# Optimization experiments

Measured on AMD Instinct MI355X. Metric: run time of the kernel, lower is better.

Reference implementation:

```python
import jax, jax.numpy as jnp
import numpy as np

N_NODES = 50000


def gcn_conv(x, src, dst, deg_inv_sqrt, W, b, n_nodes):
    # GCNConv: h = x @ W; msg = norm * h[src]; out = scatter_add(msg, dst) + b
    h = x @ W  # [N, out]
    norm = deg_inv_sqrt[src] * deg_inv_sqrt[dst]  # symmetric normalization
    msg = h[src] * norm[:, None]  # [E+N, out]
    out = jax.ops.segment_sum(msg, dst, num_segments=n_nodes)
    return out + b


def setup_inputs() -> dict:
    key = jax.random.key(0)
    k_x, k_e, k_w1, k_w2 = jax.random.split(key, 4)
    in_c, hid, out_c = 256, 64, 64
    x = jax.random.normal(k_x, (N_NODES, 256), dtype=jnp.float32)
    edge_index = jax.random.randint(k_e, (2, 1600000), 0, N_NODES, dtype=jnp.int64)
    # Glorot-ish weights, zero bias as in GCNConv defaults
    W1 = jax.random.normal(k_w1, (in_c, hid), dtype=jnp.float32) / np.sqrt(in_c)
    b1 = jnp.zeros((hid,), dtype=jnp.float32)
    W2 = jax.random.normal(k_w2, (hid, out_c), dtype=jnp.float32) / np.sqrt(hid)
    b2 = jnp.zeros((out_c,), dtype=jnp.float32)
    return {"x": x, "edge_index": edge_index, "W1": W1, "b1": b1, "W2": W2, "b2": b2}


def reference(x, edge_index, W1, b1, W2, b2):
    n = x.shape[0]
    loops = jnp.arange(n, dtype=edge_index.dtype)
    src = jnp.concatenate([edge_index[0], loops])  # add self-loops
    dst = jnp.concatenate([edge_index[1], loops])
    deg = jax.ops.segment_sum(jnp.ones_like(dst, dtype=x.dtype), dst, num_segments=n)
    deg_inv_sqrt = jnp.where(deg > 0, jax.lax.rsqrt(deg), 0.0)
    h = gcn_conv(x, src, dst, deg_inv_sqrt, W1, b1, n)
    h = jax.nn.relu(h)
    out = gcn_conv(h, src, dst, deg_inv_sqrt, W2, b2, n)
    return out
```

## Files before the change

### kernel.cpp

```cpp
#include <hip/hip_runtime.h>
#include <hip/hip_bf16.h>


#define NB_MAX 1024

__device__ inline unsigned short f2bf(float f) {
    unsigned u = __builtin_bit_cast(unsigned, f);
    return (unsigned short)((u + 0x7FFFu + ((u >> 16) & 1u)) >> 16);
}
__device__ inline float bf2f(unsigned short b) {
    return __builtin_bit_cast(float, (unsigned)b << 16);
}


__global__ __launch_bounds__(256) void k_hist(const int* __restrict__ ei, int E,
                                              int nb, int chunk,
                                              int* __restrict__ histT) {
    __shared__ int h[NB_MAX];
    for (int i = threadIdx.x; i < nb; i += 256) h[i] = 0;
    __syncthreads();
    int e0 = blockIdx.x * chunk, e1 = min(E, e0 + chunk);
    for (int e = e0 + threadIdx.x; e < e1; e += 256)
        atomicAdd(&h[ei[E + e] >> 6], 1);
    __syncthreads();
    for (int b = threadIdx.x; b < nb; b += 256)
        histT[b * 256 + blockIdx.x] = h[b];
}


__global__ __launch_bounds__(256) void k_scan_cols(int* __restrict__ histT,
                                                   int* __restrict__ total) {
    __shared__ int sm[256];
    int b = blockIdx.x, t = threadIdx.x;
    int v = histT[b * 256 + t];
    sm[t] = v;
    __syncthreads();
    for (int off = 1; off < 256; off <<= 1) {
        int u = (t >= off) ? sm[t - off] : 0;
        __syncthreads();
        sm[t] += u;
        __syncthreads();
    }
    histT[b * 256 + t] = sm[t] - v;
    if (t == 255) total[b] = sm[255];
}


__global__ __launch_bounds__(1024) void k_scan_totals(const int* __restrict__ total,
                                                      int* __restrict__ base, int nb) {
    __shared__ int sm[1024];
    int t = threadIdx.x;
    int v = (t < nb) ? total[t] : 0;
    sm[t] = v;
    __syncthreads();
    for (int off = 1; off < 1024; off <<= 1) {
        int u = (t >= off) ? sm[t - off] : 0;
        __syncthreads();
        sm[t] += u;
        __syncthreads();
    }
    if (t < nb) base[t] = sm[t] - v;
    if (t == nb - 1) base[nb] = sm[t];
}


__global__ __launch_bounds__(256) void k_scatter(const int* __restrict__ ei, int E,
                                                 int nb, int chunk,
                                                 const int* __restrict__ histT,
                                                 const int* __restrict__ base,
                                                 unsigned* __restrict__ packed) {
    __shared__ int cur[NB_MAX];
    for (int b = threadIdx.x; b < nb; b += 256)
        cur[b] = base[b] + histT[b * 256 + blockIdx.x];
    __syncthreads();
    int e0 = blockIdx.x * chunk, e1 = min(E, e0 + chunk);
    for (int e = e0 + threadIdx.x; e < e1; e += 256) {
        int s = ei[e], d = ei[E + e];
        int pos = atomicAdd(&cur[d >> 6], 1);
        packed[pos] = (unsigned)s | ((unsigned)(d & 63) << 16);
    }
}


__global__ __launch_bounds__(256) void k_csr(const unsigned* __restrict__ packed,
                                             const int* __restrict__ base,
                                             int n,
                                             int* __restrict__ qbeg,
                                             int* __restrict__ qcnt,
                                             float* __restrict__ dinv,
                                             unsigned short* __restrict__ ssrcp,
                                             unsigned short* __restrict__ hs1,
                                             unsigned short* __restrict__ hs2) {
    __shared__ int cnt[64];
    __shared__ int cur[64];
    const int b = blockIdx.x, t = threadIdx.x;
    const int p0 = base[b], p1 = base[b + 1];
    if (t < 64) cnt[t] = 0;
    __syncthreads();
    for (int p = p0 + t; p < p1; p += 256)
        atomicAdd(&cnt[(packed[p] >> 16) & 63], 1);
    __syncthreads();
    if (t < 64) {
        int deg = cnt[t];
        int pdeg = (deg + 1) & ~1;
        int sum = pdeg;
#pragma unroll
        for (int d = 1; d < 64; d <<= 1) {
            int u = __shfl_up(sum, d, 64);
            if (t >= d) sum += u;
        }
        int excl = sum - pdeg;
        int pb = (2 + p0 + 128 * b + 1) & ~1;
        int start = pb + excl;
        int node = (b << 6) + t;
        if (node < n) {
            qbeg[node] = start >> 1;
            qcnt[node] = pdeg >> 1;
            dinv[node] = 1.0f / sqrtf((float)(deg + 1));
        }
        cur[t] = start;
    }
    __syncthreads();
    for (int p = p0 + t; p < p1; p += 256) {
        unsigned k = packed[p];
        int pos = atomicAdd(&cur[(k >> 16) & 63], 1);
        ssrcp[pos] = (unsigned short)(k & 0xFFFFu);
    }
    __syncthreads();
    if (t < 64 && (cnt[t] & 1))
        ssrcp[cur[t]] = (unsigned short)n;
    if (b == 0) {
        if (t < 64) {
            hs1[(size_t)n * 64 + t] = 0;
            hs2[(size_t)n * 64 + t] = 0;
        }
        if (t == 0) {
            ssrcp[0] = (unsigned short)n;
            ssrcp[1] = (unsigned short)n;
        }
    }
}


#define FMA4(A, s, wv)                                                         \
    (A).x += (s) * (wv).x; (A).y += (s) * (wv).y;                              \
    (A).z += (s) * (wv).z; (A).w += (s) * (wv).w;

template <int K>
__global__ __launch_bounds__(256) void k_gemm(const float* __restrict__ X,
                                              const float* __restrict__ W,
                                              const float* __restrict__ dinv,
                                              unsigned short* __restrict__ HS,
                                              int n) {
    __shared__ float xl[64][36];
    __shared__ float wl[32][64];

    const int t = threadIdx.x;
    const int tc = t & 15;
    const int tr = t >> 4;
    const int row0 = blockIdx.x * 64;

    float4 acc[4];
    acc[0] = acc[1] = acc[2] = acc[3] = make_float4(0.f, 0.f, 0.f, 0.f);

    for (int k0 = 0; k0 < K; k0 += 32) {
#pragma unroll
        for (int i = 0; i < 2; ++i) {
            int idx = i * 256 + t;
            int r = idx >> 3, f4 = idx & 7;
            int gr = row0 + r;
            float4 v = make_float4(0.f, 0.f, 0.f, 0.f);
            if (gr < n) v = *(const float4*)(X + (size_t)gr * K + k0 + f4 * 4);
            *(float4*)&xl[r][f4 * 4] = v;
        }
#pragma unroll
        for (int i = 0; i < 2; ++i) {
            int idx = i * 256 + t;
            int kr = idx >> 4, f4 = idx & 15;
            *(float4*)&wl[kr][f4 * 4] =
                *(const float4*)(W + (size_t)(k0 + kr) * 64 + f4 * 4);
        }
        __syncthreads();

#pragma unroll
        for (int kk = 0; kk < 32; kk += 4) {
            float4 xv0 = *(float4*)&xl[tr * 4 + 0][kk];
            float4 xv1 = *(float4*)&xl[tr * 4 + 1][kk];
            float4 xv2 = *(float4*)&xl[tr * 4 + 2][kk];
            float4 xv3 = *(float4*)&xl[tr * 4 + 3][kk];
            float4 wv0 = *(float4*)&wl[kk + 0][tc * 4];
            float4 wv1 = *(float4*)&wl[kk + 1][tc * 4];
            float4 wv2 = *(float4*)&wl[kk + 2][tc * 4];
            float4 wv3 = *(float4*)&wl[kk + 3][tc * 4];

            FMA4(acc[0], xv0.x, wv0); FMA4(acc[0], xv0.y, wv1);
            FMA4(acc[0], xv0.z, wv2); FMA4(acc[0], xv0.w, wv3);
            FMA4(acc[1], xv1.x, wv0); FMA4(acc[1], xv1.y, wv1);
            FMA4(acc[1], xv1.z, wv2); FMA4(acc[1], xv1.w, wv3);
            FMA4(acc[2], xv2.x, wv0); FMA4(acc[2], xv2.y, wv1);
            FMA4(acc[2], xv2.z, wv2); FMA4(acc[2], xv2.w, wv3);
            FMA4(acc[3], xv3.x, wv0); FMA4(acc[3], xv3.y, wv1);
            FMA4(acc[3], xv3.z, wv2); FMA4(acc[3], xv3.w, wv3);
        }
        __syncthreads();
    }

#pragma unroll
    for (int ri = 0; ri < 4; ++ri) {
        int gr = row0 + tr * 4 + ri;
        if (gr < n) {
            float dv = dinv[gr];
            float4 o = acc[ri];
            ushort4 pk;
            pk.x = f2bf(o.x * dv); pk.y = f2bf(o.y * dv);
            pk.z = f2bf(o.z * dv); pk.w = f2bf(o.w * dv);
            *(ushort4*)(HS + (size_t)gr * 64 + tc * 4) = pk;
        }
    }
}


template <bool RELU>
__global__ void k_agg(const unsigned short* __restrict__ hs,
                      const int* __restrict__ qbeg,
                      const int* __restrict__ qcnt,
                      const unsigned short* __restrict__ ssrcp,
                      const float* __restrict__ dinv,
                      const float* __restrict__ bias,
                      float* __restrict__ out, int n) {
    int node = blockIdx.x * 4 + (threadIdx.x >> 6);
    if (node >= n) return;
    node = __builtin_amdgcn_readfirstlane(node);
    const int lane = threadIdx.x & 63;
    const int half = lane >> 5;
    const int cp   = lane & 31;

    const unsigned* hsu = (const unsigned*)hs;
    const unsigned* ssu = (const unsigned*)ssrcp;

    const int q0 = qbeg[node];
    const int m  = qcnt[node];

    const unsigned sv = hsu[node * 32 + cp];
    const float dv = dinv[node];
    const float2 bv = *(const float2*)(bias + 2 * cp);

    float ax = 0.f, ay = 0.f;
    int qb = 0;
    for (; qb + 16 <= m; qb += 16) {
        unsigned ss[16];
#pragma unroll
        for (int j = 0; j < 16; ++j) ss[j] = ssu[q0 + qb + j];
        unsigned v[16];
#pragma unroll
        for (int j = 0; j < 16; ++j) {
            int s = half ? (int)(ss[j] >> 16) : (int)(ss[j] & 0xFFFFu);
            v[j] = hsu[s * 32 + cp];
        }
#pragma unroll
        for (int j = 0; j < 16; ++j) {
            ax += __builtin_bit_cast(float, v[j] << 16);
            ay += __builtin_bit_cast(float, v[j] & 0xFFFF0000u);
        }
    }
    const int rem = m - qb;
    if (rem) {
        unsigned ss[16];
#pragma unroll
        for (int j = 0; j < 16; ++j) {
            int q = (j < rem) ? (q0 + qb + j) : 0;
            ss[j] = ssu[q];
        }
        unsigned v[16];
#pragma unroll
        for (int j = 0; j < 16; ++j) {
            int s = half ? (int)(ss[j] >> 16) : (int)(ss[j] & 0xFFFFu);
            v[j] = hsu[s * 32 + cp];
        }
#pragma unroll
        for (int j = 0; j < 16; ++j) {
            ax += __builtin_bit_cast(float, v[j] << 16);
            ay += __builtin_bit_cast(float, v[j] & 0xFFFF0000u);
        }
    }

    ax += __shfl_xor(ax, 32, 64);
    ay += __shfl_xor(ay, 32, 64);

    float rx = dv * (ax + __builtin_bit_cast(float, sv << 16)) + bv.x;
    float ry = dv * (ay + __builtin_bit_cast(float, sv & 0xFFFF0000u)) + bv.y;
    if (RELU) { rx = fmaxf(rx, 0.f); ry = fmaxf(ry, 0.f); }
    if (half == 0)
        *(float2*)(out + (size_t)node * 64 + 2 * cp) = make_float2(rx, ry);
}


extern "C" void kernel_launch(void* const* d_in, const int* in_sizes, int n_in,
                              void* d_out, int out_size, void* d_ws, size_t ws_size,
                              hipStream_t stream) {
    const float* x  = (const float*)d_in[0];
    const int*   ei = (const int*)d_in[1];
    const float* W1 = (const float*)d_in[2];
    const float* b1 = (const float*)d_in[3];
    const float* W2 = (const float*)d_in[4];
    const float* b2 = (const float*)d_in[5];

    const int n = in_sizes[0] / 256;
    const int E = in_sizes[1] / 2;
    const int nb = (n + 63) >> 6;
    const int chunk = (E + 255) / 256;

    char* ws = (char*)d_ws;
    auto carve = [&](size_t bytes) {
        void* p = (void*)ws;
        ws += (bytes + 255) & ~(size_t)255;
        return p;
    };
    int*            histT  = (int*)carve((size_t)nb * 256 * 4);
    int*            total  = (int*)carve((size_t)nb * 4);
    int*            base   = (int*)carve((size_t)(nb + 1) * 4);
    unsigned*       packed = (unsigned*)carve((size_t)E * 4);
    unsigned short* ssrcp  = (unsigned short*)carve(((size_t)E + 128 * nb + 256) * 2);
    int*            qbeg   = (int*)carve((size_t)n * 4);
    int*            qcnt   = (int*)carve((size_t)n * 4);
    float*          dinv   = (float*)carve((size_t)n * 4);
    unsigned short* hs1    = (unsigned short*)carve((size_t)(n + 1) * 64 * 2);
    float*          hB     = (float*)carve((size_t)n * 64 * 4);
    unsigned short* hs2    = (unsigned short*)carve((size_t)(n + 1) * 64 * 2);

    k_hist<<<256, 256, 0, stream>>>(ei, E, nb, chunk, histT);
    k_scan_cols<<<nb, 256, 0, stream>>>(histT, total);
    k_scan_totals<<<1, 1024, 0, stream>>>(total, base, nb);
    k_scatter<<<256, 256, 0, stream>>>(ei, E, nb, chunk, histT, base, packed);
    k_csr<<<nb, 256, 0, stream>>>(packed, base, n, qbeg, qcnt, dinv, ssrcp,
                                  hs1, hs2);

    const int nbG = (n + 63) / 64;

    k_gemm<256><<<nbG, 256, 0, stream>>>(x, W1, dinv, hs1, n);
    k_agg<true><<<(n + 3) / 4, 256, 0, stream>>>(hs1, qbeg, qcnt, ssrcp, dinv,
                                                 b1, hB, n);

    k_gemm<64><<<nbG, 256, 0, stream>>>(hB, W2, dinv, hs2, n);
    k_agg<false><<<(n + 3) / 4, 256, 0, stream>>>(hs2, qbeg, qcnt, ssrcp, dinv,
                                                  b2, (float*)d_out, n);
}
```

Before: 224.3 us.

## Use bf16 MFMA for both GEMMs and store hidden layer as bf16

Replaces the scalar FP32 tiled GEMMs with bf16 MFMA 16x16x32 kernels. Weights are pre-transposed and converted to bf16 by a small extra kernel, and X is converted to bf16 while being loaded into shared memory. The first aggregation now writes the hidden activation as bf16, which halves that intermediate's traffic and feeds the second GEMM directly. This cuts ALU work, but the lower-precision inputs add rounding error.

```diff
diff --git a/kernel.cpp b/kernel.cpp
--- a/kernel.cpp
+++ b/kernel.cpp
@@ -3,13 +3,13 @@
 
 
 #define NB_MAX 1024
+
+typedef __attribute__((ext_vector_type(8))) short bf16x8;
+typedef __attribute__((ext_vector_type(4))) float f32x4;
 
 __device__ inline unsigned short f2bf(float f) {
     unsigned u = __builtin_bit_cast(unsigned, f);
     return (unsigned short)((u + 0x7FFFu + ((u >> 16) & 1u)) >> 16);
-}
-__device__ inline float bf2f(unsigned short b) {
-    return __builtin_bit_cast(float, (unsigned)b << 16);
 }
 
 
@@ -142,92 +142,103 @@
 }
 
 
-#define FMA4(A, s, wv)                                                         \
-    (A).x += (s) * (wv).x; (A).y += (s) * (wv).y;                              \
-    (A).z += (s) * (wv).z; (A).w += (s) * (wv).w;
-
-template <int K>
-__global__ __launch_bounds__(256) void k_gemm(const float* __restrict__ X,
-                                              const float* __restrict__ W,
-                                              const float* __restrict__ dinv,
-                                              unsigned short* __restrict__ HS,
-                                              int n) {
-    __shared__ float xl[64][36];
-    __shared__ float wl[32][64];
+__global__ __launch_bounds__(256) void k_tw(const float* __restrict__ W1,
+                                            const float* __restrict__ W2,
+                                            unsigned short* __restrict__ W1T,
+                                            unsigned short* __restrict__ W2T) {
+    int t = threadIdx.x;
+    int nn = t & 63, kb = t >> 6;
+    if (blockIdx.x == 0) {
+        for (int k = kb; k < 256; k += 4)
+            W1T[nn * 256 + k] = f2bf(W1[k * 64 + nn]);
+    } else {
+        for (int k = kb; k < 64; k += 4)
+            W2T[nn * 64 + k] = f2bf(W2[k * 64 + nn]);
+    }
+}
+
+
+template <int K, bool XBF16>
+__global__ __launch_bounds__(256) void k_gemm_mfma(const void* __restrict__ Xv,
+                                                   const unsigned short* __restrict__ WT,
+                                                   const float* __restrict__ dinv,
+                                                   unsigned short* __restrict__ HS,
+                                                   int n) {
+    __shared__ unsigned short xl[64][40];
+    __shared__ unsigned short wl[64][K + 8];
 
     const int t = threadIdx.x;
-    const int tc = t & 15;
-    const int tr = t >> 4;
+    const int lane = t & 63, w = t >> 6;
+    const int m = lane & 15, quad = lane >> 4;
     const int row0 = blockIdx.x * 64;
 
-    float4 acc[4];
-    acc[0] = acc[1] = acc[2] = acc[3] = make_float4(0.f, 0.f, 0.f, 0.f);
+    for (int idx = t; idx < 64 * (K / 8); idx += 256) {
+        int r = idx / (K / 8), seg = idx % (K / 8);
+        *(uint4*)&wl[r][seg * 8] = *(const uint4*)(WT + r * K + seg * 8);
+    }
+
+    f32x4 acc[4];
+#pragma unroll
+    for (int c = 0; c < 4; ++c) acc[c] = (f32x4)(0.0f);
 
     for (int k0 = 0; k0 < K; k0 += 32) {
-#pragma unroll
-        for (int i = 0; i < 2; ++i) {
-            int idx = i * 256 + t;
-            int r = idx >> 3, f4 = idx & 7;
+        __syncthreads();
+        if (XBF16) {
+            const unsigned short* Xb = (const unsigned short*)Xv;
+            int r = t >> 2, sg = t & 3;
             int gr = row0 + r;
-            float4 v = make_float4(0.f, 0.f, 0.f, 0.f);
-            if (gr < n) v = *(const float4*)(X + (size_t)gr * K + k0 + f4 * 4);
-            *(float4*)&xl[r][f4 * 4] = v;
-        }
-#pragma unroll
-        for (int i = 0; i < 2; ++i) {
-            int idx = i * 256 + t;
-            int kr = idx >> 4, f4 = idx & 15;
-            *(float4*)&wl[kr][f4 * 4] =
-                *(const float4*)(W + (size_t)(k0 + kr) * 64 + f4 * 4);
-        }
-        __syncthreads();
-
-#pragma unroll
-        for (int kk = 0; kk < 32; kk += 4) {
-            float4 xv0 = *(float4*)&xl[tr * 4 + 0][kk];
-            float4 xv1 = *(float4*)&xl[tr * 4 + 1][kk];
-            float4 xv2 = *(float4*)&xl[tr * 4 + 2][kk];
-            float4 xv3 = *(float4*)&xl[tr * 4 + 3][kk];
-            float4 wv0 = *(float4*)&wl[kk + 0][tc * 4];
-            float4 wv1 = *(float4*)&wl[kk + 1][tc * 4];
-            float4 wv2 = *(float4*)&wl[kk + 2][tc * 4];
-            float4 wv3 = *(float4*)&wl[kk + 3][tc * 4];
-
-            FMA4(acc[0], xv0.x, wv0); FMA4(acc[0], xv0.y, wv1);
-            FMA4(acc[0], xv0.z, wv2); FMA4(acc[0], xv0.w, wv3);
-            FMA4(acc[1], xv1.x, wv0); FMA4(acc[1], xv1.y, wv1);
-            FMA4(acc[1], xv1.z, wv2); FMA4(acc[1], xv1.w, wv3);
-            FMA4(acc[2], xv2.x, wv0); FMA4(acc[2], xv2.y, wv1);
-            FMA4(acc[2], xv2.z, wv2); FMA4(acc[2], xv2.w, wv3);
-            FMA4(acc[3], xv3.x, wv0); FMA4(acc[3], xv3.y, wv1);
-            FMA4(acc[3], xv3.z, wv2); FMA4(acc[3], xv3.w, wv3);
-        }
-        __syncthreads();
-    }
-
-#pragma unroll
-    for (int ri = 0; ri < 4; ++ri) {
-        int gr = row0 + tr * 4 + ri;
-        if (gr < n) {
-            float dv = dinv[gr];
-            float4 o = acc[ri];
-            ushort4 pk;
-            pk.x = f2bf(o.x * dv); pk.y = f2bf(o.y * dv);
-            pk.z = f2bf(o.z * dv); pk.w = f2bf(o.w * dv);
-            *(ushort4*)(HS + (size_t)gr * 64 + tc * 4) = pk;
-        }
-    }
-}
-
-
-template <bool RELU>
+            uint4 v = {0u, 0u, 0u, 0u};
+            if (gr < n)
+                v = *(const uint4*)(Xb + (size_t)gr * K + k0 + sg * 8);
+            *(uint4*)&xl[r][sg * 8] = v;
+        } else {
+            const float* Xf = (const float*)Xv;
+#pragma unroll
+            for (int i = 0; i < 2; ++i) {
+                int idx = i * 256 + t;
+                int r = idx >> 3, f4 = idx & 7;
+                int gr = row0 + r;
+                float4 v = make_float4(0.f, 0.f, 0.f, 0.f);
+                if (gr < n)
+                    v = *(const float4*)(Xf + (size_t)gr * K + k0 + f4 * 4);
+                ushort4 pk;
+                pk.x = f2bf(v.x); pk.y = f2bf(v.y);
+                pk.z = f2bf(v.z); pk.w = f2bf(v.w);
+                *(ushort4*)&xl[r][f4 * 4] = pk;
+            }
+        }
+        __syncthreads();
+
+        bf16x8 aF = *(const bf16x8*)&xl[w * 16 + m][quad * 8];
+#pragma unroll
+        for (int c = 0; c < 4; ++c) {
+            bf16x8 bF = *(const bf16x8*)&wl[c * 16 + m][k0 + quad * 8];
+            acc[c] = __builtin_amdgcn_mfma_f32_16x16x32_bf16(aF, bF, acc[c],
+                                                             0, 0, 0);
+        }
+    }
+
+#pragma unroll
+    for (int reg = 0; reg < 4; ++reg) {
+        int row = row0 + w * 16 + quad * 4 + reg;
+        if (row < n) {
+            float dv = dinv[row];
+#pragma unroll
+            for (int c = 0; c < 4; ++c)
+                HS[(size_t)row * 64 + c * 16 + m] = f2bf(acc[c][reg] * dv);
+        }
+    }
+}
+
+
+template <bool L1>
 __global__ void k_agg(const unsigned short* __restrict__ hs,
                       const int* __restrict__ qbeg,
                       const int* __restrict__ qcnt,
                       const unsigned short* __restrict__ ssrcp,
                       const float* __restrict__ dinv,
                       const float* __restrict__ bias,
-                      float* __restrict__ out, int n) {
+                      void* __restrict__ outv, int n) {
     int node = blockIdx.x * 4 + (threadIdx.x >> 6);
     if (node >= n) return;
     node = __builtin_amdgcn_readfirstlane(node);
@@ -289,9 +300,16 @@
 
     float rx = dv * (ax + __builtin_bit_cast(float, sv << 16)) + bv.x;
     float ry = dv * (ay + __builtin_bit_cast(float, sv & 0xFFFF0000u)) + bv.y;
-    if (RELU) { rx = fmaxf(rx, 0.f); ry = fmaxf(ry, 0.f); }
-    if (half == 0)
-        *(float2*)(out + (size_t)node * 64 + 2 * cp) = make_float2(rx, ry);
+    if (half == 0) {
+        if (L1) {
+            rx = fmaxf(rx, 0.f); ry = fmaxf(ry, 0.f);
+            ushort2 pk; pk.x = f2bf(rx); pk.y = f2bf(ry);
+            *(ushort2*)((unsigned short*)outv + (size_t)node * 64 + 2 * cp) = pk;
+        } else {
+            *(float2*)((float*)outv + (size_t)node * 64 + 2 * cp) =
+                make_float2(rx, ry);
+        }
+    }
 }
 
 
@@ -324,8 +342,10 @@
     int*            qbeg   = (int*)carve((size_t)n * 4);
     int*            qcnt   = (int*)carve((size_t)n * 4);
     float*          dinv   = (float*)carve((size_t)n * 4);
+    unsigned short* W1T    = (unsigned short*)carve(64 * 256 * 2);
+    unsigned short* W2T    = (unsigned short*)carve(64 * 64 * 2);
     unsigned short* hs1    = (unsigned short*)carve((size_t)(n + 1) * 64 * 2);
-    float*          hB     = (float*)carve((size_t)n * 64 * 4);
+    unsigned short* hB     = (unsigned short*)carve((size_t)n * 64 * 2);
     unsigned short* hs2    = (unsigned short*)carve((size_t)(n + 1) * 64 * 2);
 
     k_hist<<<256, 256, 0, stream>>>(ei, E, nb, chunk, histT);
@@ -334,14 +354,15 @@
     k_scatter<<<256, 256, 0, stream>>>(ei, E, nb, chunk, histT, base, packed);
     k_csr<<<nb, 256, 0, stream>>>(packed, base, n, qbeg, qcnt, dinv, ssrcp,
                                   hs1, hs2);
+    k_tw<<<2, 256, 0, stream>>>(W1, W2, W1T, W2T);
 
     const int nbG = (n + 63) / 64;
 
-    k_gemm<256><<<nbG, 256, 0, stream>>>(x, W1, dinv, hs1, n);
+    k_gemm_mfma<256, false><<<nbG, 256, 0, stream>>>(x, W1T, dinv, hs1, n);
     k_agg<true><<<(n + 3) / 4, 256, 0, stream>>>(hs1, qbeg, qcnt, ssrcp, dinv,
                                                  b1, hB, n);
 
-    k_gemm<64><<<nbG, 256, 0, stream>>>(hB, W2, dinv, hs2, n);
+    k_gemm_mfma<64, true><<<nbG, 256, 0, stream>>>(hB, W2T, dinv, hs2, n);
     k_agg<false><<<(n + 3) / 4, 256, 0, stream>>>(hs2, qbeg, qcnt, ssrcp, dinv,
-                                                  b2, (float*)d_out, n);
-}
+                                                  b2, d_out, n);
+}
```

New measurement: 225.0 us. No clear change (+0.3%).
